# Kernel tuning notes

Hardware: AMD Instinct MI355X
Metric: run time of the kernel (lower is better)

The kernel has to match this reference:

```python
import jax, jax.numpy as jnp
import numpy as np

KH, KW = 3, 3
DIL = 1
PH = DIL * (KH - 1) // 2
PW = DIL * (KW - 1) // 2


def setup_inputs() -> dict:
    key = jax.random.key(0)
    kq, kk = jax.random.split(key)
    B, C, H, W = 8, 128, 128, 128
    Q = jax.random.normal(kq, (B, C, H, W), dtype=jnp.float32)
    K = jax.random.normal(kk, (B, C, H, W), dtype=jnp.float32)
    return {"Q": Q, "K": K}


def reference(Q, K):
    # output[b, i*KW+j, h, w] = sum_c Q[b,c,h,w] * K_padded[b,c,h+i*DIL, w+j*DIL]
    B, C, H, W = Q.shape
    Kp = jnp.pad(K, ((0, 0), (0, 0), (PH, PH), (PW, PW)))
    outs = []
    for i in range(KH):
        for j in range(KW):
            Ks = Kp[:, :, i * DIL:i * DIL + H, j * DIL:j * DIL + W]  # shifted K window
            outs.append(jnp.sum(Q * Ks, axis=1))  # reduce over channels -> (B,H,W)
    return jnp.stack(outs, axis=1)  # (B, KH*KW, H, W)
```

## Files before the change

### kernel.cpp

```cpp
#include <hip/hip_runtime.h>


#define Bn 8
#define Cn 128
#define Hn 128
#define Wn 128
#define HWn (Hn * Wn)
#define CSPLIT 4
#define CCHUNK (Cn / CSPLIT)
#define OUTN (Bn * 9 * HWn)

template <bool ATOMIC>
__global__ __launch_bounds__(256) void msa_conv_v4(
    const float* __restrict__ Q, const float* __restrict__ K,
    float* __restrict__ dst) {
  const int tid  = threadIdx.x;
  const int lane = tid & 63;
  const int wq   = lane & 31;
  const int rl   = lane >> 5;
  const int wv   = tid >> 6;
  const int h0   = blockIdx.x * 8;
  const int r    = h0 + wv * 2 + rl;
  const int b    = blockIdx.y;
  const int cs   = blockIdx.z;
  const int w0   = wq * 4;

  const int rm = (r > 0) ? r - 1 : r + 1;
  const int rp = (r < Hn - 1) ? r + 1 : r - 1;

  const size_t base = (size_t)b * Cn * HWn + (size_t)cs * CCHUNK * HWn;
  const float* qp = Q + base + (size_t)r  * Wn + w0;
  const float* mp = K + base + (size_t)rm * Wn + w0;
  const float* zp = K + base + (size_t)r  * Wn + w0;
  const float* pp = K + base + (size_t)rp * Wn + w0;

  float acc[9][4];
#pragma unroll
  for (int t = 0; t < 9; ++t)
#pragma unroll
    for (int k = 0; k < 4; ++k) acc[t][k] = 0.f;

#define ACC4(t, s0, s1, s2, s3) \
  acc[t][0] += q4.x * (s0);     \
  acc[t][1] += q4.y * (s1);     \
  acc[t][2] += q4.z * (s2);     \
  acc[t][3] += q4.w * (s3);

#pragma unroll 2
  for (int c = 0; c < CCHUNK; ++c) {
    const float4 q4 = *(const float4*)qp;
    const float4 m4 = *(const float4*)mp;
    const float4 z4 = *(const float4*)zp;
    const float4 p4 = *(const float4*)pp;
    const float mL = __shfl_up(m4.w, 1, 64);
    const float zL = __shfl_up(z4.w, 1, 64);
    const float pL = __shfl_up(p4.w, 1, 64);
    const float mR = __shfl_down(m4.x, 1, 64);
    const float zR = __shfl_down(z4.x, 1, 64);
    const float pR = __shfl_down(p4.x, 1, 64);

    ACC4(0, mL,   m4.x, m4.y, m4.z)
    ACC4(1, m4.x, m4.y, m4.z, m4.w)
    ACC4(2, m4.y, m4.z, m4.w, mR)
    ACC4(3, zL,   z4.x, z4.y, z4.z)
    ACC4(4, z4.x, z4.y, z4.z, z4.w)
    ACC4(5, z4.y, z4.z, z4.w, zR)
    ACC4(6, pL,   p4.x, p4.y, p4.z)
    ACC4(7, p4.x, p4.y, p4.z, p4.w)
    ACC4(8, p4.y, p4.z, p4.w, pR)

    qp += HWn; mp += HWn; zp += HWn; pp += HWn;
  }
#undef ACC4

  if (wq == 0)  { acc[0][0] = 0.f; acc[3][0] = 0.f; acc[6][0] = 0.f; }
  if (wq == 31) { acc[2][3] = 0.f; acc[5][3] = 0.f; acc[8][3] = 0.f; }
  if (r == 0) {
#pragma unroll
    for (int t = 0; t < 3; ++t)
#pragma unroll
      for (int k = 0; k < 4; ++k) acc[t][k] = 0.f;
  }
  if (r == Hn - 1) {
#pragma unroll
    for (int t = 6; t < 9; ++t)
#pragma unroll
      for (int k = 0; k < 4; ++k) acc[t][k] = 0.f;
  }

  const size_t o = (size_t)b * 9 * HWn + (size_t)r * Wn + w0;
  if (ATOMIC) {
#pragma unroll
    for (int t = 0; t < 9; ++t)
#pragma unroll
      for (int k = 0; k < 4; ++k)
        atomicAdd(dst + o + (size_t)t * HWn + k, acc[t][k]);
  } else {
    float* p = dst + (size_t)cs * OUTN + o;
#pragma unroll
    for (int t = 0; t < 9; ++t) {
      *(float4*)(p + (size_t)t * HWn) =
          make_float4(acc[t][0], acc[t][1], acc[t][2], acc[t][3]);
    }
  }
}

__global__ __launch_bounds__(256) void msa_reduce4(
    const float* __restrict__ part, float* __restrict__ out) {
  const int i = blockIdx.x * 256 + threadIdx.x;
  const float4* p = (const float4*)part;
  const int n4 = OUTN / 4;
  float4 s0 = p[i];
  float4 s1 = p[n4 + i];
  float4 s2 = p[2 * n4 + i];
  float4 s3 = p[3 * n4 + i];
  float4 r;
  r.x = (s0.x + s1.x) + (s2.x + s3.x);
  r.y = (s0.y + s1.y) + (s2.y + s3.y);
  r.z = (s0.z + s1.z) + (s2.z + s3.z);
  r.w = (s0.w + s1.w) + (s2.w + s3.w);
  ((float4*)out)[i] = r;
}

__global__ __launch_bounds__(256) void msa_zero(float* __restrict__ out) {
  const int i = blockIdx.x * 256 + threadIdx.x;
  ((float4*)out)[i] = make_float4(0.f, 0.f, 0.f, 0.f);
}

extern "C" void kernel_launch(void* const* d_in, const int* in_sizes, int n_in,
                              void* d_out, int out_size, void* d_ws,
                              size_t ws_size, hipStream_t stream) {
  const float* Q = (const float*)d_in[0];
  const float* K = (const float*)d_in[1];
  float* out = (float*)d_out;

  dim3 block(256);
  dim3 grid(Hn / 8, Bn, CSPLIT);

  const size_t ws_need = (size_t)CSPLIT * OUTN * sizeof(float);
  if (ws_size >= ws_need) {
    float* part = (float*)d_ws;
    msa_conv_v4<false><<<grid, block, 0, stream>>>(Q, K, part);
    msa_reduce4<<<OUTN / 4 / 256, 256, 0, stream>>>(part, out);
  } else {
    msa_zero<<<OUTN / 4 / 256, 256, 0, stream>>>(out);
    msa_conv_v4<true><<<grid, block, 0, stream>>>(Q, K, out);
  }
}
```

Baseline: 154.7 us.

## Stage K rows in LDS via async loads and reduce channel halves in-block

Replaces the 4-way channel-split kernel plus a separate reduction pass with one kernel per 4-row block. K halo rows are copied into double-buffered LDS with async global-to-LDS loads, overlapped with compute, and two half-block groups each reduce half the channels before combining through LDS. This removes the partial-sum workspace traffic and the second launch, and cuts redundant K row reads. In exchange the grid shrinks to 256 blocks, which may leave the GPU underoccupied, and the code depends on hand-written vmcnt waits being correct.

```diff
diff --git a/kernel.cpp b/kernel.cpp
--- a/kernel.cpp
+++ b/kernel.cpp
@@ -6,125 +6,169 @@
 #define Hn 128
 #define Wn 128
 #define HWn (Hn * Wn)
-#define CSPLIT 4
-#define CCHUNK (Cn / CSPLIT)
-#define OUTN (Bn * 9 * HWn)
+#define TC 4
+#define NCHUNK (64 / TC)
 
-template <bool ATOMIC>
-__global__ __launch_bounds__(256) void msa_conv_v4(
+__device__ __forceinline__ void async16(void* lds, const void* g) {
+  __builtin_amdgcn_global_load_lds(
+      (const __attribute__((address_space(1))) void*)g,
+      (__attribute__((address_space(3))) void*)lds, 16, 0, 0);
+}
+
+__global__ __launch_bounds__(256) void msa_conv_v5(
     const float* __restrict__ Q, const float* __restrict__ K,
-    float* __restrict__ dst) {
+    float* __restrict__ out) {
+  __shared__ float kbuf[2][TC][2][6][Wn];
+
   const int tid  = threadIdx.x;
   const int lane = tid & 63;
-  const int wq   = lane & 31;
-  const int rl   = lane >> 5;
   const int wv   = tid >> 6;
-  const int h0   = blockIdx.x * 8;
-  const int r    = h0 + wv * 2 + rl;
+  const int hh   = wv >> 1;
+  const int qpar = wv & 1;
+  const int idx  = tid & 127;
+  const int rr   = idx >> 5;
+  const int wq   = idx & 31;
+  const int w0   = wq * 4;
+  const int r0   = blockIdx.x * 4;
+  const int r    = r0 + rr;
   const int b    = blockIdx.y;
-  const int cs   = blockIdx.z;
-  const int w0   = wq * 4;
 
+  const int src0 = (r0 == 0) ? 0 : ((r0 == Hn - 4) ? (Hn - 6) : (r0 - 1));
   const int rm = (r > 0) ? r - 1 : r + 1;
   const int rp = (r < Hn - 1) ? r + 1 : r - 1;
+  const int sm = rm - src0, s0 = r - src0, sp = rp - src0;
 
-  const size_t base = (size_t)b * Cn * HWn + (size_t)cs * CCHUNK * HWn;
-  const float* qp = Q + base + (size_t)r  * Wn + w0;
-  const float* mp = K + base + (size_t)rm * Wn + w0;
-  const float* zp = K + base + (size_t)r  * Wn + w0;
-  const float* pp = K + base + (size_t)rp * Wn + w0;
+  const int offc = w0 * 4;
+  const int offl = (wq == 0) ? 0 : (offc - 4);
+  const int offr = (wq == 31) ? (offc + 12) : (offc + 16);
 
-  float acc[9][4];
-#pragma unroll
-  for (int t = 0; t < 9; ++t)
-#pragma unroll
-    for (int k = 0; k < 4; ++k) acc[t][k] = 0.f;
+  const char* kbytes = (const char*)K + (size_t)b * Cn * HWn * 4;
+  char* lds0 = (char*)&kbuf[0][0][0][0][0];
+  const float* qbase =
+      Q + ((size_t)b * Cn + (size_t)hh * 64) * HWn + (size_t)r * Wn + w0;
 
-#define ACC4(t, s0, s1, s2, s3) \
-  acc[t][0] += q4.x * (s0);     \
-  acc[t][1] += q4.y * (s1);     \
-  acc[t][2] += q4.z * (s2);     \
-  acc[t][3] += q4.w * (s3);
+  float acc[9][4] = {};
+  float4 qA[TC], qB[TC];
 
-#pragma unroll 2
-  for (int c = 0; c < CCHUNK; ++c) {
-    const float4 q4 = *(const float4*)qp;
-    const float4 m4 = *(const float4*)mp;
-    const float4 z4 = *(const float4*)zp;
-    const float4 p4 = *(const float4*)pp;
-    const float mL = __shfl_up(m4.w, 1, 64);
-    const float zL = __shfl_up(z4.w, 1, 64);
-    const float pL = __shfl_up(p4.w, 1, 64);
-    const float mR = __shfl_down(m4.x, 1, 64);
-    const float zR = __shfl_down(z4.x, 1, 64);
-    const float pR = __shfl_down(p4.x, 1, 64);
+#define STAGE(chn, bufn)                                                     \
+  do {                                                                       \
+    _Pragma("unroll") for (int j = 0; j < 2; ++j) {                          \
+      const int s = qpar + 2 * j;                                            \
+      const int c = hh * 64 + (chn) * TC + s;                                \
+      const char* src =                                                      \
+          kbytes + (size_t)c * (HWn * 4) + src0 * 512 + lane * 16;           \
+      char* dst = lds0 + (((bufn) * TC + s) * 2 + hh) * 3072 + lane * 16;    \
+      async16(dst, src);                                                     \
+      async16(dst + 1024, src + 1024);                                       \
+      async16(dst + 2048, src + 2048);                                       \
+    }                                                                        \
+  } while (0)
 
-    ACC4(0, mL,   m4.x, m4.y, m4.z)
-    ACC4(1, m4.x, m4.y, m4.z, m4.w)
-    ACC4(2, m4.y, m4.z, m4.w, mR)
-    ACC4(3, zL,   z4.x, z4.y, z4.z)
-    ACC4(4, z4.x, z4.y, z4.z, z4.w)
-    ACC4(5, z4.y, z4.z, z4.w, zR)
-    ACC4(6, pL,   p4.x, p4.y, p4.z)
-    ACC4(7, p4.x, p4.y, p4.z, p4.w)
-    ACC4(8, p4.y, p4.z, p4.w, pR)
+#define LOADQ(dst, chn)                                                      \
+  do {                                                                       \
+    const float* qp = qbase + (size_t)(chn) * TC * HWn;                      \
+    _Pragma("unroll") for (int s = 0; s < TC; ++s) dst[s] =                  \
+        *(const float4*)(qp + (size_t)s * HWn);                              \
+  } while (0)
 
-    qp += HWn; mp += HWn; zp += HWn; pp += HWn;
-  }
-#undef ACC4
+#define ROW(t0, rb)                                                          \
+  do {                                                                       \
+    const float4 kc = *(const float4*)((rb) + offc);                         \
+    const float kl = *(const float*)((rb) + offl);                           \
+    const float kr = *(const float*)((rb) + offr);                           \
+    acc[t0][0] += qv.x * kl;                                                 \
+    acc[t0][1] += qv.y * kc.x;                                               \
+    acc[t0][2] += qv.z * kc.y;                                               \
+    acc[t0][3] += qv.w * kc.z;                                               \
+    acc[t0 + 1][0] += qv.x * kc.x;                                           \
+    acc[t0 + 1][1] += qv.y * kc.y;                                           \
+    acc[t0 + 1][2] += qv.z * kc.z;                                           \
+    acc[t0 + 1][3] += qv.w * kc.w;                                           \
+    acc[t0 + 2][0] += qv.x * kc.y;                                           \
+    acc[t0 + 2][1] += qv.y * kc.z;                                           \
+    acc[t0 + 2][2] += qv.z * kc.w;                                           \
+    acc[t0 + 2][3] += qv.w * kr;                                             \
+  } while (0)
 
-  if (wq == 0)  { acc[0][0] = 0.f; acc[3][0] = 0.f; acc[6][0] = 0.f; }
-  if (wq == 31) { acc[2][3] = 0.f; acc[5][3] = 0.f; acc[8][3] = 0.f; }
-  if (r == 0) {
-#pragma unroll
-    for (int t = 0; t < 3; ++t)
-#pragma unroll
-      for (int k = 0; k < 4; ++k) acc[t][k] = 0.f;
-  }
-  if (r == Hn - 1) {
-#pragma unroll
-    for (int t = 6; t < 9; ++t)
-#pragma unroll
-      for (int k = 0; k < 4; ++k) acc[t][k] = 0.f;
+#define COMPUTE(qreg, bufn)                                                  \
+  do {                                                                       \
+    _Pragma("unroll") for (int s = 0; s < TC; ++s) {                         \
+      const char* kstep = lds0 + (((bufn) * TC + s) * 2 + hh) * 3072;        \
+      const float4 qv = qreg[s];                                             \
+      ROW(0, kstep + sm * 512);                                              \
+      ROW(3, kstep + s0 * 512);                                              \
+      ROW(6, kstep + sp * 512);                                              \
+    }                                                                        \
+  } while (0)
+
+  LOADQ(qA, 0);
+  asm volatile("" ::: "memory");
+  STAGE(0, 0);
+  asm volatile("" ::: "memory");
+
+#pragma unroll 1
+  for (int ch = 0; ch < NCHUNK; ch += 2) {
+    LOADQ(qB, ch + 1);
+    asm volatile("" ::: "memory");
+    STAGE(ch + 1, 1);
+    asm volatile("s_waitcnt vmcnt(10)" ::: "memory");
+    __builtin_amdgcn_s_barrier();
+    asm volatile("" ::: "memory");
+    COMPUTE(qA, 0);
+    asm volatile("" ::: "memory");
+    __builtin_amdgcn_s_barrier();
+
+    if (ch + 2 < NCHUNK) {
+      LOADQ(qA, ch + 2);
+      asm volatile("" ::: "memory");
+      STAGE(ch + 2, 0);
+      asm volatile("s_waitcnt vmcnt(10)" ::: "memory");
+    } else {
+      asm volatile("s_waitcnt vmcnt(0)" ::: "memory");
+    }
+    __builtin_amdgcn_s_barrier();
+    asm volatile("" ::: "memory");
+    COMPUTE(qB, 1);
+    asm volatile("" ::: "memory");
+    __builtin_amdgcn_s_barrier();
   }
 
-  const size_t o = (size_t)b * 9 * HWn + (size_t)r * Wn + w0;
-  if (ATOMIC) {
+  __syncthreads();
+  float* scr = (float*)lds0;
+  if (hh == 1) {
 #pragma unroll
     for (int t = 0; t < 9; ++t)
 #pragma unroll
-      for (int k = 0; k < 4; ++k)
-        atomicAdd(dst + o + (size_t)t * HWn + k, acc[t][k]);
-  } else {
-    float* p = dst + (size_t)cs * OUTN + o;
+      for (int k = 0; k < 4; ++k) scr[idx * 36 + t * 4 + k] = acc[t][k];
+  }
+  __syncthreads();
+  if (hh == 0) {
 #pragma unroll
-    for (int t = 0; t < 9; ++t) {
-      *(float4*)(p + (size_t)t * HWn) =
+    for (int t = 0; t < 9; ++t)
+#pragma unroll
+      for (int k = 0; k < 4; ++k) acc[t][k] += scr[idx * 36 + t * 4 + k];
+
+    if (wq == 0) { acc[0][0] = 0.f; acc[3][0] = 0.f; acc[6][0] = 0.f; }
+    if (wq == 31) { acc[2][3] = 0.f; acc[5][3] = 0.f; acc[8][3] = 0.f; }
+    if (r == 0) {
+#pragma unroll
+      for (int t = 0; t < 3; ++t)
+#pragma unroll
+        for (int k = 0; k < 4; ++k) acc[t][k] = 0.f;
+    }
+    if (r == Hn - 1) {
+#pragma unroll
+      for (int t = 6; t < 9; ++t)
+#pragma unroll
+        for (int k = 0; k < 4; ++k) acc[t][k] = 0.f;
+    }
+
+    float* o = out + (size_t)b * 9 * HWn + (size_t)r * Wn + w0;
+#pragma unroll
+    for (int t = 0; t < 9; ++t)
+      *(float4*)(o + (size_t)t * HWn) =
           make_float4(acc[t][0], acc[t][1], acc[t][2], acc[t][3]);
-    }
   }
-}
-
-__global__ __launch_bounds__(256) void msa_reduce4(
-    const float* __restrict__ part, float* __restrict__ out) {
-  const int i = blockIdx.x * 256 + threadIdx.x;
-  const float4* p = (const float4*)part;
-  const int n4 = OUTN / 4;
-  float4 s0 = p[i];
-  float4 s1 = p[n4 + i];
-  float4 s2 = p[2 * n4 + i];
-  float4 s3 = p[3 * n4 + i];
-  float4 r;
-  r.x = (s0.x + s1.x) + (s2.x + s3.x);
-  r.y = (s0.y + s1.y) + (s2.y + s3.y);
-  r.z = (s0.z + s1.z) + (s2.z + s3.z);
-  r.w = (s0.w + s1.w) + (s2.w + s3.w);
-  ((float4*)out)[i] = r;
-}
-
-__global__ __launch_bounds__(256) void msa_zero(float* __restrict__ out) {
-  const int i = blockIdx.x * 256 + threadIdx.x;
-  ((float4*)out)[i] = make_float4(0.f, 0.f, 0.f, 0.f);
 }
 
 extern "C" void kernel_launch(void* const* d_in, const int* in_sizes, int n_in,
@@ -135,15 +179,6 @@
   float* out = (float*)d_out;
 
   dim3 block(256);
-  dim3 grid(Hn / 8, Bn, CSPLIT);
-
-  const size_t ws_need = (size_t)CSPLIT * OUTN * sizeof(float);
-  if (ws_size >= ws_need) {
-    float* part = (float*)d_ws;
-    msa_conv_v4<false><<<grid, block, 0, stream>>>(Q, K, part);
-    msa_reduce4<<<OUTN / 4 / 256, 256, 0, stream>>>(part, out);
-  } else {
-    msa_zero<<<OUTN / 4 / 256, 256, 0, stream>>>(out);
-    msa_conv_v4<true><<<grid, block, 0, stream>>>(Q, K, out);
-  }
+  dim3 grid(Hn / 4, Bn);
+  msa_conv_v5<<<grid, block, 0, stream>>>(Q, K, out);
 }
```

After: 154.4 us. About the same (-0.2%).
